# Optimization experiments

Hardware: AMD Instinct MI355X
Metric: run time of the kernel (lower is better)

## Reference

```python
import jax, jax.numpy as jnp
import numpy as np

B, L, D = 32, 512, 256
MAX_DUR = 8


def setup_inputs() -> dict:
    key = jax.random.key(0)
    k1, k2 = jax.random.split(key)
    hidden_phonems = jax.random.normal(k1, (B, L, D), dtype=jnp.float32)
    durations = jax.random.randint(k2, (B, L), 0, MAX_DUR, dtype=jnp.int32)
    return {"hidden_phonems": hidden_phonems, "durations": durations}


def reference(hidden_phonems, durations):
    # hidden_phonems: [B, L, D], durations: [B, L] int
    totals = jnp.sum(durations, axis=1)                    # [B] mel length per utterance
    max_T = int(jnp.max(totals))                           # batch-max padded length (matches torch)
    cum = jnp.cumsum(durations, axis=1)                    # [B, L] exclusive-of-next prefix sums
    t = jnp.arange(max_T, dtype=jnp.int32)                 # output frame positions
    # frame t belongs to the first phoneme whose cumulative duration exceeds t
    idx = jax.vmap(lambda c: jnp.searchsorted(c, t, side='right'))(cum)  # [B, max_T]
    idx = jnp.clip(idx, 0, hidden_phonems.shape[1] - 1)
    out = jnp.take_along_axis(hidden_phonems, idx[:, :, None], axis=1)   # [B, max_T, D]
    mask = (t[None, :] < totals[:, None])                  # zero out padding frames
    return out * mask[:, :, None].astype(out.dtype)
```

## Files before the change

kernel.cpp:

```cpp
#include <hip/hip_runtime.h>
#include <hip/hip_bf16.h>

#define B_SZ 32
#define L_SZ 512
#define D_SZ 256
#define PHON_PER_WAVE 2
#define PHON_BLOCKS (B_SZ * L_SZ / (4 * PHON_PER_WAVE))
#define PAD_FRAMES_PER_BLOCK 64

__global__ void __launch_bounds__(256)
lr_kernel(const float* __restrict__ hidden,
          const int* __restrict__ durations,
          float* __restrict__ out,
          int maxT, int padBlocksPerB) {
    const int tid  = threadIdx.x;
    const int lane = tid & 63;
    const int wave = tid >> 6;

    if (blockIdx.x < PHON_BLOCKS) {
        const int wid  = blockIdx.x * 4 + wave;
        const int b    = wid >> 8;
        const int l0   = (wid & 255) * 2;
        const int l1   = l0 + 1;

        const float4* src0 =
            (const float4*)(hidden + ((size_t)(b * L_SZ + l0)) * D_SZ);
        const float4* src1 =
            (const float4*)(hidden + ((size_t)(b * L_SZ + l1)) * D_SZ);
        const float4 v0 = src0[lane];
        const float4 v1 = src1[lane];

        const int4* drow = (const int4*)(durations + b * L_SZ);
        const int4 a = drow[lane * 2];
        const int4 c = drow[lane * 2 + 1];

        const int base = lane * 8;
        int s = 0;
        s += (base + 0 < l0) ? a.x : 0;
        s += (base + 1 < l0) ? a.y : 0;
        s += (base + 2 < l0) ? a.z : 0;
        s += (base + 3 < l0) ? a.w : 0;
        s += (base + 4 < l0) ? c.x : 0;
        s += (base + 5 < l0) ? c.y : 0;
        s += (base + 6 < l0) ? c.z : 0;
        s += (base + 7 < l0) ? c.w : 0;
        #pragma unroll
        for (int off = 32; off; off >>= 1) s += __shfl_xor(s, off, 64);
        const int start0 = s;

        const int k = l0 & 7;
        const int p0 =
            (k < 4) ? (k == 0 ? a.x : a.z) : (k == 4 ? c.x : c.z);
        const int p1 =
            (k < 4) ? (k == 0 ? a.y : a.w) : (k == 4 ? c.y : c.w);
        const int d0 = __shfl(p0, l0 >> 3, 64);
        const int d1 = __shfl(p1, l0 >> 3, 64);
        const int start1 = start0 + d0;

        float4* dst0 =
            (float4*)(out + ((size_t)b * maxT + start0) * D_SZ) + lane;
        float4* dst1 =
            (float4*)(out + ((size_t)b * maxT + start1) * D_SZ) + lane;
        #pragma unroll
        for (int j = 0; j < 7; ++j) {
            if (j < d0) dst0[j * 64] = v0;
            if (j < d1) dst1[j * 64] = v1;
        }
    } else {
        const int pb   = blockIdx.x - PHON_BLOCKS;
        const int b    = pb / padBlocksPerB;
        const int tile = pb % padBlocksPerB;
        const int t0   = tile * PAD_FRAMES_PER_BLOCK;

        const int4* drow = (const int4*)(durations + b * L_SZ);
        const int4 a = drow[lane * 2];
        const int4 c = drow[lane * 2 + 1];
        int s = a.x + a.y + a.z + a.w + c.x + c.y + c.z + c.w;
        #pragma unroll
        for (int off = 32; off; off >>= 1) s += __shfl_xor(s, off, 64);
        const int total = s;

        if (t0 + PAD_FRAMES_PER_BLOCK <= total) return;

        const float4 z = make_float4(0.f, 0.f, 0.f, 0.f);
        const int tw = t0 + wave * (PAD_FRAMES_PER_BLOCK / 4);
        #pragma unroll
        for (int i = 0; i < PAD_FRAMES_PER_BLOCK / 4; ++i) {
            const int t = tw + i;
            if (t >= total && t < maxT) {
                float4* dst = (float4*)(out + ((size_t)b * maxT + t) * D_SZ);
                dst[lane] = z;
            }
        }
    }
}

extern "C" void kernel_launch(void* const* d_in, const int* in_sizes, int n_in,
                              void* d_out, int out_size, void* d_ws, size_t ws_size,
                              hipStream_t stream) {
    const float* hidden = (const float*)d_in[0];
    const int* durations = (const int*)d_in[1];
    float* out = (float*)d_out;

    const int maxT = out_size / (B_SZ * D_SZ);
    const int padBlocksPerB = (maxT + PAD_FRAMES_PER_BLOCK - 1) / PAD_FRAMES_PER_BLOCK;
    const int grid = PHON_BLOCKS + B_SZ * padBlocksPerB;

    lr_kernel<<<grid, 256, 0, stream>>>(hidden, durations, out,
                                        maxT, padBlocksPerB);
}
```

Baseline: 81.99 us.

## Fuse padding zero-fill into phoneme blocks and pack prefix/total reduction

Removes the separate padding-block branch. Each phoneme wave now also zero-fills padding frames in a strided loop, using the utterance total. The total and the prefix start are computed in a single wave reduction by packing them into the low and high 16-bit halves of one int, which relies on sums fitting in 16 bits. This shrinks the grid and drops the duplicate duration loads and reductions the pad blocks did, at the cost of extra work inside the phoneme blocks.

```diff
diff --git a/kernel.cpp b/kernel.cpp
--- a/kernel.cpp
+++ b/kernel.cpp
@@ -6,92 +6,66 @@
 #define D_SZ 256
 #define PHON_PER_WAVE 2
 #define PHON_BLOCKS (B_SZ * L_SZ / (4 * PHON_PER_WAVE))
-#define PAD_FRAMES_PER_BLOCK 64
 
 __global__ void __launch_bounds__(256)
 lr_kernel(const float* __restrict__ hidden,
           const int* __restrict__ durations,
           float* __restrict__ out,
-          int maxT, int padBlocksPerB) {
+          int maxT) {
     const int tid  = threadIdx.x;
     const int lane = tid & 63;
     const int wave = tid >> 6;
 
-    if (blockIdx.x < PHON_BLOCKS) {
-        const int wid  = blockIdx.x * 4 + wave;
-        const int b    = wid >> 8;
-        const int l0   = (wid & 255) * 2;
-        const int l1   = l0 + 1;
+    const int wid = blockIdx.x * 4 + wave;
+    const int b   = wid >> 8;
+    const int w   = wid & 255;
+    const int l0  = w * 2;
 
-        const float4* src0 =
-            (const float4*)(hidden + ((size_t)(b * L_SZ + l0)) * D_SZ);
-        const float4* src1 =
-            (const float4*)(hidden + ((size_t)(b * L_SZ + l1)) * D_SZ);
-        const float4 v0 = src0[lane];
-        const float4 v1 = src1[lane];
+    const float4* src0 =
+        (const float4*)(hidden + ((size_t)(b * L_SZ + l0)) * D_SZ);
+    const float4 v0 = src0[lane];
+    const float4 v1 = src0[lane + 64];
 
-        const int4* drow = (const int4*)(durations + b * L_SZ);
-        const int4 a = drow[lane * 2];
-        const int4 c = drow[lane * 2 + 1];
+    const int4* drow = (const int4*)(durations + b * L_SZ);
+    const int4 a = drow[lane * 2];
+    const int4 c = drow[lane * 2 + 1];
 
-        const int base = lane * 8;
-        int s = 0;
-        s += (base + 0 < l0) ? a.x : 0;
-        s += (base + 1 < l0) ? a.y : 0;
-        s += (base + 2 < l0) ? a.z : 0;
-        s += (base + 3 < l0) ? a.w : 0;
-        s += (base + 4 < l0) ? c.x : 0;
-        s += (base + 5 < l0) ? c.y : 0;
-        s += (base + 6 < l0) ? c.z : 0;
-        s += (base + 7 < l0) ? c.w : 0;
-        #pragma unroll
-        for (int off = 32; off; off >>= 1) s += __shfl_xor(s, off, 64);
-        const int start0 = s;
+    const int base = lane * 8;
+    int p = 0;
+    p += ((base + 0 < l0) ? a.x : 0) + (a.x << 16);
+    p += ((base + 1 < l0) ? a.y : 0) + (a.y << 16);
+    p += ((base + 2 < l0) ? a.z : 0) + (a.z << 16);
+    p += ((base + 3 < l0) ? a.w : 0) + (a.w << 16);
+    p += ((base + 4 < l0) ? c.x : 0) + (c.x << 16);
+    p += ((base + 5 < l0) ? c.y : 0) + (c.y << 16);
+    p += ((base + 6 < l0) ? c.z : 0) + (c.z << 16);
+    p += ((base + 7 < l0) ? c.w : 0) + (c.w << 16);
+    #pragma unroll
+    for (int off = 32; off; off >>= 1) p += __shfl_xor(p, off, 64);
+    const int start0 = p & 0xffff;
+    const int total  = ((unsigned)p) >> 16;
 
-        const int k = l0 & 7;
-        const int p0 =
-            (k < 4) ? (k == 0 ? a.x : a.z) : (k == 4 ? c.x : c.z);
-        const int p1 =
-            (k < 4) ? (k == 0 ? a.y : a.w) : (k == 4 ? c.y : c.w);
-        const int d0 = __shfl(p0, l0 >> 3, 64);
-        const int d1 = __shfl(p1, l0 >> 3, 64);
-        const int start1 = start0 + d0;
+    const int k = l0 & 7;
+    const int p0 = (k < 4) ? (k == 0 ? a.x : a.z) : (k == 4 ? c.x : c.z);
+    const int p1 = (k < 4) ? (k == 0 ? a.y : a.w) : (k == 4 ? c.y : c.w);
+    const int d0 = __shfl(p0, l0 >> 3, 64);
+    const int d1 = __shfl(p1, l0 >> 3, 64);
+    const int start1 = start0 + d0;
 
-        float4* dst0 =
-            (float4*)(out + ((size_t)b * maxT + start0) * D_SZ) + lane;
-        float4* dst1 =
-            (float4*)(out + ((size_t)b * maxT + start1) * D_SZ) + lane;
-        #pragma unroll
-        for (int j = 0; j < 7; ++j) {
-            if (j < d0) dst0[j * 64] = v0;
-            if (j < d1) dst1[j * 64] = v1;
-        }
-    } else {
-        const int pb   = blockIdx.x - PHON_BLOCKS;
-        const int b    = pb / padBlocksPerB;
-        const int tile = pb % padBlocksPerB;
-        const int t0   = tile * PAD_FRAMES_PER_BLOCK;
+    float4* dst0 =
+        (float4*)(out + ((size_t)b * maxT + start0) * D_SZ) + lane;
+    float4* dst1 =
+        (float4*)(out + ((size_t)b * maxT + start1) * D_SZ) + lane;
+    #pragma unroll
+    for (int j = 0; j < 7; ++j) {
+        if (j < d0) dst0[j * 64] = v0;
+        if (j < d1) dst1[j * 64] = v1;
+    }
 
-        const int4* drow = (const int4*)(durations + b * L_SZ);
-        const int4 a = drow[lane * 2];
-        const int4 c = drow[lane * 2 + 1];
-        int s = a.x + a.y + a.z + a.w + c.x + c.y + c.z + c.w;
-        #pragma unroll
-        for (int off = 32; off; off >>= 1) s += __shfl_xor(s, off, 64);
-        const int total = s;
-
-        if (t0 + PAD_FRAMES_PER_BLOCK <= total) return;
-
-        const float4 z = make_float4(0.f, 0.f, 0.f, 0.f);
-        const int tw = t0 + wave * (PAD_FRAMES_PER_BLOCK / 4);
-        #pragma unroll
-        for (int i = 0; i < PAD_FRAMES_PER_BLOCK / 4; ++i) {
-            const int t = tw + i;
-            if (t >= total && t < maxT) {
-                float4* dst = (float4*)(out + ((size_t)b * maxT + t) * D_SZ);
-                dst[lane] = z;
-            }
-        }
+    const float4 z = make_float4(0.f, 0.f, 0.f, 0.f);
+    for (int t = total + w; t < maxT; t += 256) {
+        float4* dst = (float4*)(out + ((size_t)b * maxT + t) * D_SZ);
+        dst[lane] = z;
     }
 }
 
@@ -103,9 +77,6 @@
     float* out = (float*)d_out;
 
     const int maxT = out_size / (B_SZ * D_SZ);
-    const int padBlocksPerB = (maxT + PAD_FRAMES_PER_BLOCK - 1) / PAD_FRAMES_PER_BLOCK;
-    const int grid = PHON_BLOCKS + B_SZ * padBlocksPerB;
 
-    lr_kernel<<<grid, 256, 0, stream>>>(hidden, durations, out,
-                                        maxT, padBlocksPerB);
+    lr_kernel<<<PHON_BLOCKS, 256, 0, stream>>>(hidden, durations, out, maxT);
 }
```

Result: no change. 81.85 us (-0.2%).
